# Kernel tuning notes

Hardware: AMD Instinct MI355X
Metric: run time of the kernel (lower is better)

## Reference

```python
import jax, jax.numpy as jnp
import numpy as np

EPS = 1e-12          # sinkhorn_knopp epsilon
LOW, HIGH = 0.02, 0.98  # SquashedSigmoid bounds
N_ITERS = 10         # num_iterations
BATCH = 2097152


def setup_inputs() -> dict:
    key = jax.random.key(0)
    ks = jax.random.split(key, 9)
    dims = [6, 64, 32, 16, 9]
    inp = {"margins": jax.random.uniform(ks[0], (BATCH, 6), jnp.float32, 0.05, 1.0)}
    for i in range(4):
        fi, fo = dims[i], dims[i + 1]
        inp[f"W{i+1}"] = jax.random.normal(ks[1 + 2 * i], (fi, fo), jnp.float32) / np.float32(np.sqrt(fi))
        inp[f"b{i+1}"] = jnp.zeros((fo,), jnp.float32)
    return inp


def _mlp(x, W1, b1, W2, b2, W3, b3, W4, b4):
    h = jax.nn.relu(x @ W1 + b1)
    h = jax.nn.relu(h @ W2 + b2)
    h = jax.nn.relu(h @ W3 + b3)
    return h @ W4 + b4  # [B, 9]


def _tau(p4):
    # user-supplied tau: 4 positive params -> 3x3 matrix; 2x2 block padded with ones
    B = p4.shape[0]
    A = jnp.ones((B, 3, 3), p4.dtype)
    return A.at[:, :2, :2].set(p4.reshape(B, 2, 2))


def _sinkhorn_knopp(A, r, c):
    # batched row/col balancing; per-sample A is 3x3, r/c are length-3 margins
    for _ in range(N_ITERS):
        A = A * (r[:, :, None] / (A.sum(axis=2, keepdims=True) + EPS))
        A = A * (c[:, None, :] / (A.sum(axis=1, keepdims=True) + EPS))
    return A


def reference(margins, W1, b1, W2, b2, W3, b3, W4, b4):
    B = margins.shape[0]
    M, F = margins[:, 0:3], margins[:, 3:6]
    pars = _mlp(margins, W1, b1, W2, b2, W3, b3, W4, b4)
    muc = _tau(jnp.exp(pars[:, 0:4]))                     # [B,3,3]
    sqs = lambda x: LOW + (HIGH - LOW) * jax.nn.sigmoid(x)
    shm, shf = sqs(pars[:, 4:6]), sqs(pars[:, 6:8])
    V = jnp.exp(pars[:, -1])                              # [B]
    ones = jnp.ones((B, 1), margins.dtype)
    shm0 = jnp.concatenate([shm, ones], axis=1)           # [B,3]
    shf0 = jnp.concatenate([shf, ones], axis=1)
    mucm0, muc0f = M * shm0, F * shf0                     # row / col margins
    mum0, mu0f = M * (1 - shm0), F * (1 - shf0)
    muc = _sinkhorn_knopp(muc, mucm0, muc0f)              # [B,3,3]
    top = jnp.concatenate([muc, mum0[:, :, None]], axis=2)                    # [B,3,4]
    bot = jnp.concatenate([mu0f[:, None, :], jnp.zeros((B, 1, 1), margins.dtype)], axis=2)  # [B,1,4]
    mus = jnp.concatenate([top, bot], axis=1)             # [B,4,4]
    return (mus, V)
```

## Files before the change

### kernel.cpp

```cpp
#include <hip/hip_runtime.h>

typedef _Float16 f16x8 __attribute__((ext_vector_type(8)));
typedef float    f32x4 __attribute__((ext_vector_type(4)));

static constexpr float kLOW  = 0.02f;
static constexpr float kHIGH = 0.98f;

__device__ __forceinline__ float fast_sigmoid(float v) {
    return 1.0f / (1.0f + __expf(-v));
}
__device__ __forceinline__ float fast_rcp(float v) {
    return __builtin_amdgcn_rcpf(v);
}

__global__ __launch_bounds__(256, 4) void sinkhorn_mlp_mfma(
    const float* __restrict__ margins,
    const float* __restrict__ W1, const float* __restrict__ b1,
    const float* __restrict__ W2, const float* __restrict__ b2,
    const float* __restrict__ W3, const float* __restrict__ b3,
    const float* __restrict__ W4, const float* __restrict__ b4,
    float* __restrict__ out_mus, float* __restrict__ out_V, int B)
{
    __shared__ __align__(16) char smem_all[4 * 9216];
    const int lane = threadIdx.x & 63;
    const int wid  = threadIdx.x >> 6;
    char* smem = smem_all + wid * 9216;

    const int n16 = lane & 15;
    const int q   = lane >> 4;

    const int row  = blockIdx.x * 256 + wid * 64 + lane;
    const int rowC = row < B ? row : (B - 1);

    f16x8 B2f[2][2];
#pragma unroll
    for (int kt = 0; kt < 2; ++kt)
#pragma unroll
        for (int nt = 0; nt < 2; ++nt)
#pragma unroll
            for (int j = 0; j < 8; ++j)
                B2f[kt][nt][j] = (_Float16)W2[(kt*32 + q*8 + j)*32 + nt*16 + n16];

    f16x8 B3f;
#pragma unroll
    for (int j = 0; j < 8; ++j)
        B3f[j] = (_Float16)W3[(q*8 + j)*16 + n16];

    const float bias2_0 = b2[n16];
    const float bias2_1 = b2[16 + n16];
    const float bias3   = b3[n16];

    float x[6];
    {
        const float* mp = margins + (size_t)rowC * 6;
#pragma unroll
        for (int i = 0; i < 6; ++i) x[i] = mp[i];
    }

    {
        char* rp = smem + lane * 144;
#pragma unroll
        for (int c = 0; c < 8; ++c) {
            f16x8 hv;
#pragma unroll
            for (int k = 0; k < 8; ++k) {
                const int col = c * 8 + k;
                float a = fmaf(x[0], W1[col], b1[col]);
#pragma unroll
                for (int i = 1; i < 6; ++i) a = fmaf(x[i], W1[i * 64 + col], a);
                hv[k] = (_Float16)fmaxf(a, 0.0f);
            }
            *(f16x8*)(rp + c * 16) = hv;
        }
    }

    f16x8 A2[4][2];
#pragma unroll
    for (int mt = 0; mt < 4; ++mt)
#pragma unroll
        for (int kt = 0; kt < 2; ++kt)
            A2[mt][kt] = *(const f16x8*)(smem + (mt*16 + n16)*144 + kt*64 + q*16);

#pragma unroll
    for (int mt = 0; mt < 4; ++mt) {
#pragma unroll
        for (int nt = 0; nt < 2; ++nt) {
            f32x4 C;
            const float bb = nt ? bias2_1 : bias2_0;
            C[0] = bb; C[1] = bb; C[2] = bb; C[3] = bb;
            C = __builtin_amdgcn_mfma_f32_16x16x32_f16(A2[mt][0], B2f[0][nt], C, 0, 0, 0);
            C = __builtin_amdgcn_mfma_f32_16x16x32_f16(A2[mt][1], B2f[1][nt], C, 0, 0, 0);
            const int row0 = mt*16 + q*4;
            char* base = smem + (size_t)(nt*16 + n16) * 2;
#pragma unroll
            for (int r = 0; r < 4; ++r)
                *(_Float16*)(base + (row0 + r) * 80) = (_Float16)fmaxf(C[r], 0.0f);
        }
    }

    f16x8 A3[4];
#pragma unroll
    for (int mt = 0; mt < 4; ++mt)
        A3[mt] = *(const f16x8*)(smem + (mt*16 + n16)*80 + q*16);

#pragma unroll
    for (int mt = 0; mt < 4; ++mt) {
        f32x4 C;
        C[0] = bias3; C[1] = bias3; C[2] = bias3; C[3] = bias3;
        C = __builtin_amdgcn_mfma_f32_16x16x32_f16(A3[mt], B3f, C, 0, 0, 0);
        const int row0 = mt*16 + q*4;
#pragma unroll
        for (int r = 0; r < 4; ++r)
            *(float*)(smem + (row0 + r) * 80 + n16 * 4) = fmaxf(C[r], 0.0f);
    }

    float h3[16];
    {
        const char* rp = smem + lane * 80;
#pragma unroll
        for (int i = 0; i < 4; ++i)
            *(f32x4*)&h3[4*i] = *(const f32x4*)(rp + i * 16);
    }

    float p[9];
#pragma unroll
    for (int k = 0; k < 9; ++k) p[k] = fmaf(h3[0], W4[k], b4[k]);
#pragma unroll
    for (int j = 1; j < 16; ++j) {
        const float hj = h3[j];
        const float* w = W4 + j * 9;
#pragma unroll
        for (int k = 0; k < 9; ++k) p[k] = fmaf(hj, w[k], p[k]);
    }

    const float K00 = __expf(p[0]), K01 = __expf(p[1]);
    const float K10 = __expf(p[2]), K11 = __expf(p[3]);

    const float sh_m0 = kLOW + (kHIGH - kLOW) * fast_sigmoid(p[4]);
    const float sh_m1 = kLOW + (kHIGH - kLOW) * fast_sigmoid(p[5]);
    const float sh_f0 = kLOW + (kHIGH - kLOW) * fast_sigmoid(p[6]);
    const float sh_f1 = kLOW + (kHIGH - kLOW) * fast_sigmoid(p[7]);
    const float V = __expf(p[8]);

    const float M0 = x[0], M1 = x[1], M2 = x[2];
    const float F0 = x[3], F1 = x[4], F2 = x[5];

    const float r0 = M0 * sh_m0, r1 = M1 * sh_m1, r2 = M2;
    const float c0 = F0 * sh_f0, c1 = F1 * sh_f1, c2 = F2;
    const float mum0_0 = M0 * (1.0f - sh_m0), mum0_1 = M1 * (1.0f - sh_m1);
    const float mu0f_0 = F0 * (1.0f - sh_f0), mu0f_1 = F1 * (1.0f - sh_f1);

    float u0, u1, u2;
    float v0 = 1.0f, v1 = 1.0f, v2 = 1.0f;
#pragma unroll
    for (int it = 0; it < 10; ++it) {
        const float s0 = fmaf(K00, v0, fmaf(K01, v1, v2));
        const float s1 = fmaf(K10, v0, fmaf(K11, v1, v2));
        const float s2 = v0 + v1 + v2;
        u0 = r0 * fast_rcp(s0);
        u1 = r1 * fast_rcp(s1);
        u2 = r2 * fast_rcp(s2);
        const float t0 = fmaf(K00, u0, fmaf(K10, u1, u2));
        const float t1 = fmaf(K01, u0, fmaf(K11, u1, u2));
        const float t2 = u0 + u1 + u2;
        v0 = c0 * fast_rcp(t0);
        v1 = c1 * fast_rcp(t1);
        v2 = c2 * fast_rcp(t2);
    }
    const float A00 = u0 * K00 * v0, A01 = u0 * K01 * v1, A02 = u0 * v2;
    const float A10 = u1 * K10 * v0, A11 = u1 * K11 * v1, A12 = u1 * v2;
    const float A20 = u2 * v0,       A21 = u2 * v1,       A22 = u2 * v2;

    if (row < B) {
        float4* o = (float4*)(out_mus + (size_t)row * 16);
        o[0] = make_float4(A00, A01, A02, mum0_0);
        o[1] = make_float4(A10, A11, A12, mum0_1);
        o[2] = make_float4(A20, A21, A22, 0.0f);
        o[3] = make_float4(mu0f_0, mu0f_1, 0.0f, 0.0f);
        out_V[row] = V;
    }
}

extern "C" void kernel_launch(void* const* d_in, const int* in_sizes, int n_in,
                              void* d_out, int out_size, void* d_ws, size_t ws_size,
                              hipStream_t stream) {
    const float* margins = (const float*)d_in[0];
    const float* W1 = (const float*)d_in[1];
    const float* b1 = (const float*)d_in[2];
    const float* W2 = (const float*)d_in[3];
    const float* b2 = (const float*)d_in[4];
    const float* W3 = (const float*)d_in[5];
    const float* b3 = (const float*)d_in[6];
    const float* W4 = (const float*)d_in[7];
    const float* b4 = (const float*)d_in[8];

    const int B = in_sizes[0] / 6;
    float* out_mus = (float*)d_out;
    float* out_V   = out_mus + (size_t)B * 16;

    dim3 block(256);
    dim3 grid((B + 255) / 256);
    hipLaunchKernelGGL(sinkhorn_mlp_mfma, grid, block, 0, stream,
                       margins, W1, b1, W2, b2, W3, b3, W4, b4,
                       out_mus, out_V, B);
}
```

Measured before the change: 228.9 us.

## Move layer-1 to MFMA, transpose layer layouts, normalize Sinkhorn scaling

Layer 1 (6->64) now runs on MFMA instead of scalar FMAs, with the input row staged in LDS as a zero-padded f16 operand. All layers are recomputed in transposed form (weights as the A operand, activations as B), so biases load as vectors and results are stored as vector LDS writes. The Sinkhorn loop fixes v2=1 through a scale-invariant normalization, which removes one reciprocal per iteration, and a final full iteration restores the true scaling. Layer 1 now also rounds to f16, which adds precision risk, and the LDS layout changes could introduce bank conflicts.

Measured after the change: 227.1 us. No clear change (-0.8%).

```diff
diff --git a/kernel.cpp b/kernel.cpp
--- a/kernel.cpp
+++ b/kernel.cpp
@@ -1,6 +1,7 @@
 #include <hip/hip_runtime.h>
 
 typedef _Float16 f16x8 __attribute__((ext_vector_type(8)));
+typedef _Float16 f16x4 __attribute__((ext_vector_type(4)));
 typedef float    f32x4 __attribute__((ext_vector_type(4)));
 
 static constexpr float kLOW  = 0.02f;
@@ -32,86 +33,115 @@
     const int row  = blockIdx.x * 256 + wid * 64 + lane;
     const int rowC = row < B ? row : (B - 1);
 
-    f16x8 B2f[2][2];
-#pragma unroll
-    for (int kt = 0; kt < 2; ++kt)
-#pragma unroll
-        for (int nt = 0; nt < 2; ++nt)
+    float x[6];
+    {
+        const float* mp = margins + (size_t)rowC * 6;
+#pragma unroll
+        for (int i = 0; i < 6; ++i) x[i] = mp[i];
+    }
+
+    {
+        f16x8 xr;
+#pragma unroll
+        for (int j = 0; j < 8; ++j) xr[j] = (_Float16)0.0f;
+#pragma unroll
+        for (int i = 0; i < 6; ++i) xr[i] = (_Float16)x[i];
+        *(f16x8*)(smem + 8176 + lane * 16) = xr;
+        if (lane == 0) {
+            f16x8 z;
+#pragma unroll
+            for (int j = 0; j < 8; ++j) z[j] = (_Float16)0.0f;
+            *(f16x8*)(smem + 9200) = z;
+        }
+    }
+
+    f16x8 A1[4];
+#pragma unroll
+    for (int mt = 0; mt < 4; ++mt)
+#pragma unroll
+        for (int j = 0; j < 8; ++j) A1[mt][j] = (_Float16)0.0f;
+    if (q == 0) {
+#pragma unroll
+        for (int mt = 0; mt < 4; ++mt)
+#pragma unroll
+            for (int j = 0; j < 6; ++j)
+                A1[mt][j] = (_Float16)W1[j * 64 + mt * 16 + n16];
+    }
+
+    f16x8 A2w[2][2];
+#pragma unroll
+    for (int mt = 0; mt < 2; ++mt)
+#pragma unroll
+        for (int kt = 0; kt < 2; ++kt)
 #pragma unroll
             for (int j = 0; j < 8; ++j)
-                B2f[kt][nt][j] = (_Float16)W2[(kt*32 + q*8 + j)*32 + nt*16 + n16];
-
-    f16x8 B3f;
+                A2w[mt][kt][j] = (_Float16)W2[(kt*32 + q*8 + j)*32 + mt*16 + n16];
+
+    f16x8 A3w;
 #pragma unroll
     for (int j = 0; j < 8; ++j)
-        B3f[j] = (_Float16)W3[(q*8 + j)*16 + n16];
-
-    const float bias2_0 = b2[n16];
-    const float bias2_1 = b2[16 + n16];
-    const float bias3   = b3[n16];
-
-    float x[6];
-    {
-        const float* mp = margins + (size_t)rowC * 6;
-#pragma unroll
-        for (int i = 0; i < 6; ++i) x[i] = mp[i];
-    }
-
-    {
-        char* rp = smem + lane * 144;
-#pragma unroll
-        for (int c = 0; c < 8; ++c) {
-            f16x8 hv;
-#pragma unroll
-            for (int k = 0; k < 8; ++k) {
-                const int col = c * 8 + k;
-                float a = fmaf(x[0], W1[col], b1[col]);
-#pragma unroll
-                for (int i = 1; i < 6; ++i) a = fmaf(x[i], W1[i * 64 + col], a);
-                hv[k] = (_Float16)fmaxf(a, 0.0f);
-            }
-            *(f16x8*)(rp + c * 16) = hv;
+        A3w[j] = (_Float16)W3[(q*8 + j)*16 + n16];
+
+    f32x4 b1v[4], b2v[2], b3v;
+#pragma unroll
+    for (int mt = 0; mt < 4; ++mt) b1v[mt] = *(const f32x4*)(b1 + mt*16 + q*4);
+#pragma unroll
+    for (int mt = 0; mt < 2; ++mt) b2v[mt] = *(const f32x4*)(b2 + mt*16 + q*4);
+    b3v = *(const f32x4*)(b3 + q*4);
+
+    f16x8 BX[4];
+    {
+        const int xo   = (q == 0) ? (8176 + n16 * 16) : 9200;
+        const int step = (q == 0) ? 256 : 0;
+#pragma unroll
+        for (int nt = 0; nt < 4; ++nt)
+            BX[nt] = *(const f16x8*)(smem + xo + nt * step);
+    }
+#pragma unroll
+    for (int mt = 0; mt < 4; ++mt) {
+#pragma unroll
+        for (int nt = 0; nt < 4; ++nt) {
+            f32x4 C = b1v[mt];
+            C = __builtin_amdgcn_mfma_f32_16x16x32_f16(A1[mt], BX[nt], C, 0, 0, 0);
+            f16x4 hv;
+#pragma unroll
+            for (int r = 0; r < 4; ++r) hv[r] = (_Float16)fmaxf(C[r], 0.0f);
+            *(f16x4*)(smem + (nt*16 + n16) * 144 + mt*32 + q*8) = hv;
         }
     }
 
-    f16x8 A2[4][2];
-#pragma unroll
-    for (int mt = 0; mt < 4; ++mt)
+    f16x8 H1f[4][2];
+#pragma unroll
+    for (int nt = 0; nt < 4; ++nt)
 #pragma unroll
         for (int kt = 0; kt < 2; ++kt)
-            A2[mt][kt] = *(const f16x8*)(smem + (mt*16 + n16)*144 + kt*64 + q*16);
-
-#pragma unroll
-    for (int mt = 0; mt < 4; ++mt) {
-#pragma unroll
-        for (int nt = 0; nt < 2; ++nt) {
-            f32x4 C;
-            const float bb = nt ? bias2_1 : bias2_0;
-            C[0] = bb; C[1] = bb; C[2] = bb; C[3] = bb;
-            C = __builtin_amdgcn_mfma_f32_16x16x32_f16(A2[mt][0], B2f[0][nt], C, 0, 0, 0);
-            C = __builtin_amdgcn_mfma_f32_16x16x32_f16(A2[mt][1], B2f[1][nt], C, 0, 0, 0);
-            const int row0 = mt*16 + q*4;
-            char* base = smem + (size_t)(nt*16 + n16) * 2;
-#pragma unroll
-            for (int r = 0; r < 4; ++r)
-                *(_Float16*)(base + (row0 + r) * 80) = (_Float16)fmaxf(C[r], 0.0f);
+            H1f[nt][kt] = *(const f16x8*)(smem + (nt*16 + n16) * 144 + kt*64 + q*16);
+#pragma unroll
+    for (int mt = 0; mt < 2; ++mt) {
+#pragma unroll
+        for (int nt = 0; nt < 4; ++nt) {
+            f32x4 C = b2v[mt];
+            C = __builtin_amdgcn_mfma_f32_16x16x32_f16(A2w[mt][0], H1f[nt][0], C, 0, 0, 0);
+            C = __builtin_amdgcn_mfma_f32_16x16x32_f16(A2w[mt][1], H1f[nt][1], C, 0, 0, 0);
+            f16x4 hv;
+#pragma unroll
+            for (int r = 0; r < 4; ++r) hv[r] = (_Float16)fmaxf(C[r], 0.0f);
+            *(f16x4*)(smem + (nt*16 + n16) * 80 + mt*32 + q*8) = hv;
         }
     }
 
-    f16x8 A3[4];
-#pragma unroll
-    for (int mt = 0; mt < 4; ++mt)
-        A3[mt] = *(const f16x8*)(smem + (mt*16 + n16)*80 + q*16);
-
-#pragma unroll
-    for (int mt = 0; mt < 4; ++mt) {
-        f32x4 C;
-        C[0] = bias3; C[1] = bias3; C[2] = bias3; C[3] = bias3;
-        C = __builtin_amdgcn_mfma_f32_16x16x32_f16(A3[mt], B3f, C, 0, 0, 0);
-        const int row0 = mt*16 + q*4;
-#pragma unroll
-        for (int r = 0; r < 4; ++r)
-            *(float*)(smem + (row0 + r) * 80 + n16 * 4) = fmaxf(C[r], 0.0f);
+    f16x8 H2f[4];
+#pragma unroll
+    for (int nt = 0; nt < 4; ++nt)
+        H2f[nt] = *(const f16x8*)(smem + (nt*16 + n16) * 80 + q*16);
+#pragma unroll
+    for (int nt = 0; nt < 4; ++nt) {
+        f32x4 C = b3v;
+        C = __builtin_amdgcn_mfma_f32_16x16x32_f16(A3w, H2f[nt], C, 0, 0, 0);
+        f32x4 o;
+#pragma unroll
+        for (int r = 0; r < 4; ++r) o[r] = fmaxf(C[r], 0.0f);
+        *(f32x4*)(smem + (nt*16 + n16) * 80 + q*16) = o;
     }
 
     float h3[16];
@@ -150,26 +180,42 @@
     const float mum0_0 = M0 * (1.0f - sh_m0), mum0_1 = M1 * (1.0f - sh_m1);
     const float mu0f_0 = F0 * (1.0f - sh_f0), mu0f_1 = F1 * (1.0f - sh_f1);
 
+    const float rc2 = fast_rcp(c2);
+    const float g0 = c0 * rc2, g1 = c1 * rc2;
+    float v0 = 1.0f, v1 = 1.0f;
     float u0, u1, u2;
-    float v0 = 1.0f, v1 = 1.0f, v2 = 1.0f;
-#pragma unroll
-    for (int it = 0; it < 10; ++it) {
-        const float s0 = fmaf(K00, v0, fmaf(K01, v1, v2));
-        const float s1 = fmaf(K10, v0, fmaf(K11, v1, v2));
-        const float s2 = v0 + v1 + v2;
+#pragma unroll
+    for (int it = 0; it < 9; ++it) {
+        const float s0 = fmaf(K00, v0, fmaf(K01, v1, 1.0f));
+        const float s1 = fmaf(K10, v0, fmaf(K11, v1, 1.0f));
+        const float s2 = v0 + v1 + 1.0f;
         u0 = r0 * fast_rcp(s0);
         u1 = r1 * fast_rcp(s1);
         u2 = r2 * fast_rcp(s2);
         const float t0 = fmaf(K00, u0, fmaf(K10, u1, u2));
         const float t1 = fmaf(K01, u0, fmaf(K11, u1, u2));
         const float t2 = u0 + u1 + u2;
-        v0 = c0 * fast_rcp(t0);
-        v1 = c1 * fast_rcp(t1);
-        v2 = c2 * fast_rcp(t2);
-    }
-    const float A00 = u0 * K00 * v0, A01 = u0 * K01 * v1, A02 = u0 * v2;
-    const float A10 = u1 * K10 * v0, A11 = u1 * K11 * v1, A12 = u1 * v2;
-    const float A20 = u2 * v0,       A21 = u2 * v1,       A22 = u2 * v2;
+        v0 = g0 * (t2 * fast_rcp(t0));
+        v1 = g1 * (t2 * fast_rcp(t1));
+    }
+    float vf0, vf1, vf2;
+    {
+        const float s0 = fmaf(K00, v0, fmaf(K01, v1, 1.0f));
+        const float s1 = fmaf(K10, v0, fmaf(K11, v1, 1.0f));
+        const float s2 = v0 + v1 + 1.0f;
+        u0 = r0 * fast_rcp(s0);
+        u1 = r1 * fast_rcp(s1);
+        u2 = r2 * fast_rcp(s2);
+        const float t0 = fmaf(K00, u0, fmaf(K10, u1, u2));
+        const float t1 = fmaf(K01, u0, fmaf(K11, u1, u2));
+        const float t2 = u0 + u1 + u2;
+        vf0 = c0 * fast_rcp(t0);
+        vf1 = c1 * fast_rcp(t1);
+        vf2 = c2 * fast_rcp(t2);
+    }
+    const float A00 = u0 * K00 * vf0, A01 = u0 * K01 * vf1, A02 = u0 * vf2;
+    const float A10 = u1 * K10 * vf0, A11 = u1 * K11 * vf1, A12 = u1 * vf2;
+    const float A20 = u2 * vf0,       A21 = u2 * vf1,       A22 = u2 * vf2;
 
     if (row < B) {
         float4* o = (float4*)(out_mus + (size_t)row * 16);
```
